# Optimization experiments

Measured on AMD Instinct MI355X. Metric: run time of the kernel, lower is better.

Reference implementation:

```python
import jax, jax.numpy as jnp
import numpy as np

B, N = 16, 128
DN0, DE0, DH = 64, 16, 128  # input node dim, input edge dim, hidden dim


def _gnn2(A, x, e, w_msg, b_msg, w_node, b_node):
    """One GNN2 layer on dense batched graphs.
    A: [B,N,N] adjacency mask, x: [B,N,Dn], e: [B,N,N,De].
    Message/new-edge: relu(Linear([x_i, x_j, e_ij])) masked by A.
    New node: relu(Linear([x, sum_j msg_ij])).
    The concat-Linear is decomposed into three matmuls to avoid
    materializing the [B,N,N,2Dn+De] concat tensor.
    """
    Dn = x.shape[-1]
    Wi, Wj, We = w_msg[:Dn], w_msg[Dn:2 * Dn], w_msg[2 * Dn:]
    xi = x @ Wi                                   # [B,N,Do]
    xj = x @ Wj                                   # [B,N,Do]
    msg = jax.nn.relu(xi[:, :, None, :] + xj[:, None, :, :] + e @ We + b_msg)
    msg = msg * A[..., None]                      # mask non-edges -> new edge_attr [B,N,N,Do]
    agg = msg.sum(axis=2)                         # scatter-sum over neighbors j -> [B,N,Do]
    Wx, Wa = w_node[:Dn], w_node[Dn:]
    x_new = jax.nn.relu(x @ Wx + agg @ Wa + b_node)
    return x_new, msg


def setup_inputs() -> dict:
    key = jax.random.key(0)
    ks = iter(jax.random.split(key, 32))
    s = 0.05
    inp = {
        "edge_index": jax.random.randint(next(ks), (B, N, N), 0, 2, dtype=jnp.int32),
        "x": jax.random.normal(next(ks), (B, N, DN0), dtype=jnp.float32),
        "edge_attr": jax.random.normal(next(ks), (B, N, N, DE0), dtype=jnp.float32),
    }
    def w(shape):
        return s * jax.random.normal(next(ks), shape, dtype=jnp.float32)
    # layer 0: node_in=64, edge_in=16 -> 128
    inp["w_msg_0"], inp["b_msg_0"] = w((2 * DN0 + DE0, DH)), w((DH,))
    inp["w_node_0"], inp["b_node_0"] = w((DN0 + DH, DH)), w((DH,))
    # layers 1,2: 128 -> 128
    for l in (1, 2):
        inp[f"w_msg_{l}"], inp[f"b_msg_{l}"] = w((2 * DH + DH, DH)), w((DH,))
        inp[f"w_node_{l}"], inp[f"b_node_{l}"] = w((DH + DH, DH)), w((DH,))
    # head mlp: 128 -> 128 -> 128 -> 1
    inp["w_h1"], inp["b_h1"] = w((DH, DH)), w((DH,))
    inp["w_h2"], inp["b_h2"] = w((DH, DH)), w((DH,))
    inp["w_h3"], inp["b_h3"] = w((DH, 1)), w((1,))
    return inp


def reference(edge_index, x, edge_attr,
              w_msg_0, b_msg_0, w_node_0, b_node_0,
              w_msg_1, b_msg_1, w_node_1, b_node_1,
              w_msg_2, b_msg_2, w_node_2, b_node_2,
              w_h1, b_h1, w_h2, b_h2, w_h3, b_h3):
    A = edge_index.astype(jnp.float32)
    x = x.astype(jnp.float32)
    # layer 0
    x, e = _gnn2(A, x, edge_attr, w_msg_0, b_msg_0, w_node_0, b_node_0)
    # middle layer with 0.5 residual blend
    x_, e_ = _gnn2(A, x, e, w_msg_1, b_msg_1, w_node_1, b_node_1)
    x = 0.5 * (x + x_)
    e = 0.5 * (e + e_)
    # last layer
    x, e = _gnn2(A, x, e, w_msg_2, b_msg_2, w_node_2, b_node_2)
    # edge_mean readout + MLP head
    h = e.mean(axis=(1, 2))                       # [B, DH]
    h = jax.nn.relu(h @ w_h1 + b_h1)
    h = jax.nn.relu(h @ w_h2 + b_h2)
    out = h @ w_h3 + b_h3                         # [B, 1]
    return out.squeeze(-1)                        # [B]
```

## Files before the change

### kernel.cpp

```cpp
#include <hip/hip_runtime.h>

constexpr int B = 16, N = 128, D = 128, DN0 = 64, DE0 = 16;

typedef _Float16 half8 __attribute__((ext_vector_type(8)));
typedef _Float16 half4 __attribute__((ext_vector_type(4)));
typedef float floatx4 __attribute__((ext_vector_type(4)));
typedef float floatx16 __attribute__((ext_vector_type(16)));

__device__ __forceinline__ void gld16(const _Float16* g, _Float16* l) {
  __builtin_amdgcn_global_load_lds(
      (const __attribute__((address_space(1))) void*)g,
      (__attribute__((address_space(3))) void*)l, 16, 0, 0);
}

__global__ __launch_bounds__(128) void k_wprep(
    const float* __restrict__ wm1, const float* __restrict__ wm2,
    _Float16* __restrict__ weT1, _Float16* __restrict__ weT2) {
  const int bid = blockIdx.x;
  const int layer = bid >> 7, c = bid & 127;
  const int k = threadIdx.x;
  const float* src = layer ? wm2 : wm1;
  _Float16* dst = layer ? weT2 : weT1;
  dst[c * D + k] = (_Float16)src[(2 * D + k) * D + c];
}

__global__ __launch_bounds__(128) void k_pre0(
    const float* __restrict__ x, const float* __restrict__ wm0,
    const float* __restrict__ bm0,
    float* __restrict__ xi0, float* __restrict__ xj0) {
  const int row = blockIdx.x;
  const int c = threadIdx.x;
  __shared__ float xr[DN0];
  if (c < DN0) xr[c] = x[row * DN0 + c];
  __syncthreads();
  float ai = bm0[c], aj = 0.f;
  #pragma unroll 8
  for (int k = 0; k < DN0; ++k) {
    const float xv = xr[k];
    ai = fmaf(xv, wm0[k * D + c], ai);
    aj = fmaf(xv, wm0[(DN0 + k) * D + c], aj);
  }
  xi0[row * D + c] = ai;
  xj0[row * D + c] = aj;
}

__global__ __launch_bounds__(256) void k_edge0(
    const int* __restrict__ ei, const float* __restrict__ eattr,
    const float* __restrict__ wm0, const float* __restrict__ x0,
    const float* __restrict__ xi0, const float* __restrict__ xj0,
    const float* __restrict__ wn0, const float* __restrict__ bn0,
    const float* __restrict__ wm1, const float* __restrict__ bm1,
    _Float16* __restrict__ msg0, float* __restrict__ x1,
    float* __restrict__ xi1, float* __restrict__ xj1) {
  const int row = blockIdx.x;
  const int b = row >> 7;
  const int t = threadIdx.x;
  const int c4 = (t & 31) * 4, jb = t >> 5;

  __shared__ float e_row[N][20];
  __shared__ float w_t[DE0][D];
  __shared__ float amask[N];
  __shared__ float xi_r[D];
  __shared__ float hp2[8][32][4];
  __shared__ float sX0[DN0], sAgg[D], sX1[D];

  const float4* esrc = (const float4*)(eattr + (size_t)row * N * DE0);
  const float4* wsrc = (const float4*)(wm0 + 2 * DN0 * D);
  #pragma unroll
  for (int u = 0; u < 2; ++u) {
    const int idx4 = u * 256 + t;
    const int j = idx4 >> 2;
    const int k4 = (idx4 & 3) * 4;
    *(float4*)&e_row[j][k4] = esrc[idx4];
    ((float4*)&w_t[0][0])[idx4] = wsrc[idx4];
  }
  if (t < N) {
    amask[t] = (float)ei[(size_t)row * N + t];
    xi_r[t] = xi0[row * D + t];
  } else if (t < N + DN0) {
    sX0[t - N] = x0[(size_t)row * DN0 + (t - N)];
  }
  __syncthreads();

  float acc[16][4] = {};
  #pragma unroll 4
  for (int k = 0; k < DE0; ++k) {
    float av[16];
    #pragma unroll
    for (int p = 0; p < 16; ++p) av[p] = e_row[jb + 8 * p][k];
    const floatx4 wv = *(const floatx4*)&w_t[k][c4];
    #pragma unroll
    for (int p = 0; p < 16; ++p)
      #pragma unroll
      for (int q = 0; q < 4; ++q)
        acc[p][q] = fmaf(av[p], wv[q], acc[p][q]);
  }

  float hq[4] = {};
  const float* xjb = xj0 + (size_t)b * N * D;
  _Float16* mrow = msg0 + (size_t)row * N * D;
  const floatx4 xiv = *(const floatx4*)&xi_r[c4];
  #pragma unroll
  for (int p = 0; p < 16; ++p) {
    const int j = jb + 8 * p;
    const float am = amask[j];
    const floatx4 xjv = *(const floatx4*)&xjb[j * D + c4];
    half4 hv;
    #pragma unroll
    for (int q = 0; q < 4; ++q) {
      float v = xiv[q] + xjv[q] + acc[p][q];
      v = fmaxf(v, 0.f) * am;
      hv[q] = (_Float16)v;
      hq[q] += v;
    }
    const int cell = (c4 >> 3) ^ (j & 15);
    *(half4*)&mrow[j * D + cell * 8 + (c4 & 7)] = hv;
  }
  #pragma unroll
  for (int q = 0; q < 4; ++q) hp2[jb][t & 31][q] = hq[q];
  __syncthreads();
  if (t < D) {
    float s = 0.f;
    #pragma unroll
    for (int g = 0; g < 8; ++g) s += hp2[g][t >> 2][t & 3];
    sAgg[t] = s;
  }
  __syncthreads();

  if (t < D) {
    const int c = t;
    float a = bn0[c];
    #pragma unroll 8
    for (int k = 0; k < DN0; ++k) a = fmaf(sX0[k], wn0[k * D + c], a);
    #pragma unroll 8
    for (int k = 0; k < D; ++k) a = fmaf(sAgg[k], wn0[(DN0 + k) * D + c], a);
    a = fmaxf(a, 0.f);
    x1[(size_t)row * D + c] = a;
    sX1[c] = a;
  }
  __syncthreads();
  if (t < D) {
    const int c = t;
    float ai = bm1[c], aj = 0.f;
    #pragma unroll 8
    for (int k = 0; k < D; ++k) {
      const float xv = sX1[k];
      ai = fmaf(xv, wm1[k * D + c], ai);
      aj = fmaf(xv, wm1[(D + k) * D + c], aj);
    }
    xi1[(size_t)row * D + c] = ai;
    xj1[(size_t)row * D + c] = aj;
  }
}

__global__ __launch_bounds__(256, 4) void k_mid(
    const int* __restrict__ ei, const _Float16* __restrict__ weT1,
    const _Float16* __restrict__ weT2,
    const float* __restrict__ xi, const float* __restrict__ xj,
    const float* __restrict__ x1,
    const float* __restrict__ wn1, const float* __restrict__ bn1,
    const float* __restrict__ wm2, const float* __restrict__ bm2,
    _Float16* __restrict__ em,
    float* __restrict__ xi2, float* __restrict__ xj2) {
  const int row = blockIdx.x;
  const int b = row >> 7;
  const int t = threadIdx.x;
  const int w = t >> 6;
  const int lane = t & 63;
  const int l31 = lane & 31;
  const int l15 = lane & 15;
  const int hl = lane >> 5;

  __shared__ _Float16 sE[N * D];
  __shared__ float sAgg[D], sX1[D], sX2[D];

  const _Float16* gsrc = em + (size_t)row * N * D;
  #pragma unroll
  for (int u = 0; u < 8; ++u) {
    const int seg = (u * 4 + w) * 512;
    gld16(gsrc + seg + lane * 8, &sE[seg]);
  }

  half8 a1[8];
  #pragma unroll
  for (int ks = 0; ks < 8; ++ks)
    a1[ks] = *(const half8*)(weT1 + (32 * w + l31) * D + 16 * ks + 8 * hl);

  floatx4 xiv[4];
  #pragma unroll
  for (int g = 0; g < 4; ++g)
    xiv[g] = *(const floatx4*)&xi[(size_t)row * D + 32 * w + 8 * g + 4 * hl];
  float am[4];
  #pragma unroll
  for (int jt = 0; jt < 4; ++jt)
    am[jt] = (float)ei[(size_t)row * N + 32 * jt + l31];
  if (t < D) sX1[t] = x1[(size_t)row * D + t];

  __syncthreads();

  const floatx16 vzero = {0.f,0.f,0.f,0.f,0.f,0.f,0.f,0.f,
                          0.f,0.f,0.f,0.f,0.f,0.f,0.f,0.f};
  floatx16 acc[4];
  #pragma unroll
  for (int jt = 0; jt < 4; ++jt) acc[jt] = vzero;
  #pragma unroll
  for (int ks = 0; ks < 8; ++ks)
    #pragma unroll
    for (int jt = 0; jt < 4; ++jt) {
      const half8 bv = *(const half8*)
          &sE[(32 * jt + l31) * D + (((2 * ks + hl) ^ l15) << 3)];
      acc[jt] = __builtin_amdgcn_mfma_f32_32x32x16_f16(a1[ks], bv, acc[jt], 0, 0, 0);
    }

  __syncthreads();

  const float* xjb = xj + (size_t)b * N * D;
  floatx4 hacc[4];
  #pragma unroll
  for (int g = 0; g < 4; ++g) hacc[g] = (floatx4){0.f, 0.f, 0.f, 0.f};
  #pragma unroll
  for (int jt = 0; jt < 4; ++jt) {
    const int j = 32 * jt + l31;
    #pragma unroll
    for (int g = 0; g < 4; ++g) {
      const int cofs = 32 * w + 8 * g + 4 * hl;
      const int hidx = j * D + (((4 * w + g) ^ l15) << 3) + 4 * hl;
      const floatx4 xjv = *(const floatx4*)&xjb[j * D + cofs];
      const half4 m0 = *(const half4*)&sE[hidx];
      half4 mid;
      floatx4 m1;
      #pragma unroll
      for (int r = 0; r < 4; ++r) {
        const float v = xiv[g][r] + xjv[r] + acc[jt][4 * g + r];
        m1[r] = fmaxf(v, 0.f) * am[jt];
        mid[r] = (_Float16)(0.5f * ((float)m0[r] + m1[r]));
      }
      *(half4*)&sE[hidx] = mid;
      hacc[g] += m1;
    }
  }

  #pragma unroll
  for (int m = 1; m < 32; m <<= 1)
    #pragma unroll
    for (int g = 0; g < 4; ++g)
      #pragma unroll
      for (int r = 0; r < 4; ++r)
        hacc[g][r] += __shfl_xor(hacc[g][r], m, 64);
  if (l31 == 0) {
    #pragma unroll
    for (int g = 0; g < 4; ++g)
      *(floatx4*)&sAgg[32 * w + 8 * g + 4 * hl] = hacc[g];
  }

  half8 a2[8];
  #pragma unroll
  for (int ks = 0; ks < 8; ++ks)
    a2[ks] = *(const half8*)(weT2 + (32 * w + l31) * D + 16 * ks + 8 * hl);

  __syncthreads();

  #pragma unroll
  for (int jt = 0; jt < 4; ++jt) acc[jt] = vzero;
  #pragma unroll
  for (int ks = 0; ks < 8; ++ks)
    #pragma unroll
    for (int jt = 0; jt < 4; ++jt) {
      const half8 bv = *(const half8*)
          &sE[(32 * jt + l31) * D + (((2 * ks + hl) ^ l15) << 3)];
      acc[jt] = __builtin_amdgcn_mfma_f32_32x32x16_f16(a2[ks], bv, acc[jt], 0, 0, 0);
    }

  __syncthreads();

  #pragma unroll
  for (int jt = 0; jt < 4; ++jt) {
    const int j = 32 * jt + l31;
    #pragma unroll
    for (int g = 0; g < 4; ++g) {
      const int hidx = j * D + (((4 * w + g) ^ l15) << 3) + 4 * hl;
      half4 tv;
      #pragma unroll
      for (int r = 0; r < 4; ++r) tv[r] = (_Float16)acc[jt][4 * g + r];
      *(half4*)&sE[hidx] = tv;
    }
  }

  __syncthreads();

  uint4* gdst = (uint4*)(em + (size_t)row * N * D);
  const uint4* ls = (const uint4*)sE;
  #pragma unroll
  for (int u = 0; u < 8; ++u) {
    const int idx4 = u * 256 + t;
    gdst[idx4] = ls[idx4];
  }

  if (t < D) {
    const int c = t;
    float a = bn1[c];
    #pragma unroll 8
    for (int k = 0; k < D; ++k) a = fmaf(sX1[k], wn1[k * D + c], a);
    #pragma unroll 8
    for (int k = 0; k < D; ++k) a = fmaf(sAgg[k], wn1[(D + k) * D + c], a);
    sX2[c] = 0.5f * (sX1[c] + fmaxf(a, 0.f));
  }
  __syncthreads();
  if (t < D) {
    const int c = t;
    float ai = bm2[c], aj = 0.f;
    #pragma unroll 8
    for (int k = 0; k < D; ++k) {
      const float xv = sX2[k];
      ai = fmaf(xv, wm2[k * D + c], ai);
      aj = fmaf(xv, wm2[(D + k) * D + c], aj);
    }
    xi2[(size_t)row * D + c] = ai;
    xj2[(size_t)row * D + c] = aj;
  }
}

__global__ __launch_bounds__(256) void k_fin(
    const int* __restrict__ ei, const _Float16* __restrict__ t2,
    const float* __restrict__ xi, const float* __restrict__ xj,
    float* __restrict__ rowsum) {
  const int row = blockIdx.x;
  const int b = row >> 7;
  const int t = threadIdx.x;
  const int c8 = (t & 15) * 8, jr = t >> 4;

  __shared__ float sMask[N];
  __shared__ float hp[16][16][8];
  if (t < N) sMask[t] = (float)ei[(size_t)row * N + t];
  float xiv[8];
  *(floatx4*)&xiv[0] = *(const floatx4*)&xi[row * D + c8];
  *(floatx4*)&xiv[4] = *(const floatx4*)&xi[row * D + c8 + 4];
  __syncthreads();

  const _Float16* src = t2 + (size_t)row * N * D;
  const float* xjb = xj + (size_t)b * N * D;
  float acc8[8] = {};
  #pragma unroll
  for (int u = 0; u < 8; ++u) {
    const int j = u * 16 + jr;
    const half8 tv = *(const half8*)(src + j * D + (((t & 15) ^ jr) << 3));
    const float am = sMask[j];
    const floatx4 xj0 = *(const floatx4*)&xjb[j * D + c8];
    const floatx4 xj1 = *(const floatx4*)&xjb[j * D + c8 + 4];
    #pragma unroll
    for (int r = 0; r < 4; ++r) {
      acc8[r]     += fmaxf(xiv[r] + xj0[r] + (float)tv[r], 0.f) * am;
      acc8[4 + r] += fmaxf(xiv[4 + r] + xj1[r] + (float)tv[4 + r], 0.f) * am;
    }
  }
  #pragma unroll
  for (int k = 0; k < 8; ++k) hp[jr][t & 15][k] = acc8[k];
  __syncthreads();
  if (t < D) {
    float s = 0.f;
    #pragma unroll
    for (int g = 0; g < 16; ++g) s += hp[g][t >> 3][t & 7];
    rowsum[row * D + t] = s;
  }
}

__global__ __launch_bounds__(128) void k_head(
    const float* __restrict__ rowsum,
    const float* __restrict__ w1, const float* __restrict__ b1,
    const float* __restrict__ w2, const float* __restrict__ b2,
    const float* __restrict__ w3, const float* __restrict__ b3,
    float* __restrict__ out) {
  const int b = blockIdx.x;
  const int c = threadIdx.x;
  __shared__ float hr[D], h1r[D], h2r[D];
  const float* rs = rowsum + (size_t)b * N * D;
  float s = 0.f;
  for (int i = 0; i < N; ++i) s += rs[i * D + c];
  hr[c] = s * (1.f / (N * N));
  __syncthreads();
  float a = b1[c];
  #pragma unroll 8
  for (int k = 0; k < D; ++k) a = fmaf(hr[k], w1[k * D + c], a);
  h1r[c] = fmaxf(a, 0.f);
  __syncthreads();
  a = b2[c];
  #pragma unroll 8
  for (int k = 0; k < D; ++k) a = fmaf(h1r[k], w2[k * D + c], a);
  h2r[c] = fmaxf(a, 0.f);
  __syncthreads();
  hr[c] = h2r[c] * w3[c];
  __syncthreads();
  if (c == 0) {
    float s2 = b3[0];
    for (int k = 0; k < D; ++k) s2 += hr[k];
    out[b] = s2;
  }
}

extern "C" void kernel_launch(void* const* d_in, const int* in_sizes, int n_in,
                              void* d_out, int out_size, void* d_ws, size_t ws_size,
                              hipStream_t stream) {
  const int*   ei  = (const int*)d_in[0];
  const float* x0  = (const float*)d_in[1];
  const float* ea  = (const float*)d_in[2];
  const float* wm0 = (const float*)d_in[3];
  const float* bm0 = (const float*)d_in[4];
  const float* wn0 = (const float*)d_in[5];
  const float* bn0 = (const float*)d_in[6];
  const float* wm1 = (const float*)d_in[7];
  const float* bm1 = (const float*)d_in[8];
  const float* wn1 = (const float*)d_in[9];
  const float* bn1 = (const float*)d_in[10];
  const float* wm2 = (const float*)d_in[11];
  const float* bm2 = (const float*)d_in[12];
  const float* wh1 = (const float*)d_in[15];
  const float* bh1 = (const float*)d_in[16];
  const float* wh2 = (const float*)d_in[17];
  const float* bh2 = (const float*)d_in[18];
  const float* wh3 = (const float*)d_in[19];
  const float* bh3 = (const float*)d_in[20];
  float* out = (float*)d_out;

  _Float16* msg0h = (_Float16*)d_ws;
  _Float16* weT1  = msg0h + (size_t)B * N * N * D;
  _Float16* weT2  = weT1 + D * D;
  float* f = (float*)(weT2 + D * D);
  size_t off = 0;
  const size_t R = (size_t)B * N * D;
  float* xi0  = f + off; off += R;
  float* xj0  = f + off; off += R;
  float* x1   = f + off; off += R;
  float* xi1  = f + off; off += R;
  float* xj1  = f + off; off += R;
  float* xi2  = f + off; off += R;
  float* xj2  = f + off; off += R;
  float* rsum = f + off; off += R;

  const int rows = B * N;
  k_wprep<<<256, 128, 0, stream>>>(wm1, wm2, weT1, weT2);
  k_pre0 <<<rows, 128, 0, stream>>>(x0, wm0, bm0, xi0, xj0);
  k_edge0<<<rows, 256, 0, stream>>>(ei, ea, wm0, x0, xi0, xj0,
                                    wn0, bn0, wm1, bm1,
                                    msg0h, x1, xi1, xj1);
  k_mid  <<<rows, 256, 0, stream>>>(ei, weT1, weT2, xi1, xj1, x1,
                                    wn1, bn1, wm2, bm2,
                                    msg0h, xi2, xj2);
  k_fin  <<<rows, 256, 0, stream>>>(ei, msg0h, xi2, xj2, rsum);
  k_head <<<B,    128, 0, stream>>>(rsum, wh1, bh1, wh2, bh2, wh3, bh3, out);
}
```

Measured before the change: 261.5 us.

## Split layer-1 node update out of k_mid into a separate k_node1 kernel

Moves the per-row node update and the layer-2 xi/xj projections out of the edge-heavy k_mid kernel into a new lightweight kernel, passing the aggregated messages through a global buffer. The aim is to keep k_mid's tail, where only half the threads ran serial FMA loops, from holding the large LDS allocation and stalling the MFMA phase of the next block. Launch bounds for k_mid also drop from 4 to 2 waves per EU, giving the compiler more register room. The cost is an extra kernel launch and a global round-trip for agg1.

```diff
diff --git a/kernel.cpp b/kernel.cpp
--- a/kernel.cpp
+++ b/kernel.cpp
@@ -153,15 +153,41 @@
   }
 }
 
-__global__ __launch_bounds__(256, 4) void k_mid(
+__global__ __launch_bounds__(128) void k_node1(
+    const float* __restrict__ x1, const float* __restrict__ agg1,
+    const float* __restrict__ wn1, const float* __restrict__ bn1,
+    const float* __restrict__ wm2, const float* __restrict__ bm2,
+    float* __restrict__ xi2, float* __restrict__ xj2) {
+  const int row = blockIdx.x;
+  const int c = threadIdx.x;
+  __shared__ float x1r[D], ar[D], x2r[D];
+  x1r[c] = x1[row * D + c];
+  ar[c] = agg1[row * D + c];
+  __syncthreads();
+  float a = bn1[c];
+  #pragma unroll 8
+  for (int k = 0; k < D; ++k) a = fmaf(x1r[k], wn1[k * D + c], a);
+  #pragma unroll 8
+  for (int k = 0; k < D; ++k) a = fmaf(ar[k], wn1[(D + k) * D + c], a);
+  x2r[c] = 0.5f * (x1r[c] + fmaxf(a, 0.f));
+  __syncthreads();
+  float ai = bm2[c], aj = 0.f;
+  #pragma unroll 8
+  for (int k = 0; k < D; ++k) {
+    const float xv = x2r[k];
+    ai = fmaf(xv, wm2[k * D + c], ai);
+    aj = fmaf(xv, wm2[(D + k) * D + c], aj);
+  }
+  xi2[row * D + c] = ai;
+  xj2[row * D + c] = aj;
+}
+
+__global__ __launch_bounds__(256, 2) void k_mid(
     const int* __restrict__ ei, const _Float16* __restrict__ weT1,
     const _Float16* __restrict__ weT2,
     const float* __restrict__ xi, const float* __restrict__ xj,
-    const float* __restrict__ x1,
-    const float* __restrict__ wn1, const float* __restrict__ bn1,
-    const float* __restrict__ wm2, const float* __restrict__ bm2,
     _Float16* __restrict__ em,
-    float* __restrict__ xi2, float* __restrict__ xj2) {
+    float* __restrict__ agg1) {
   const int row = blockIdx.x;
   const int b = row >> 7;
   const int t = threadIdx.x;
@@ -172,7 +198,6 @@
   const int hl = lane >> 5;
 
   __shared__ _Float16 sE[N * D];
-  __shared__ float sAgg[D], sX1[D], sX2[D];
 
   const _Float16* gsrc = em + (size_t)row * N * D;
   #pragma unroll
@@ -194,7 +219,6 @@
   #pragma unroll
   for (int jt = 0; jt < 4; ++jt)
     am[jt] = (float)ei[(size_t)row * N + 32 * jt + l31];
-  if (t < D) sX1[t] = x1[(size_t)row * D + t];
 
   __syncthreads();
 
@@ -250,7 +274,7 @@
   if (l31 == 0) {
     #pragma unroll
     for (int g = 0; g < 4; ++g)
-      *(floatx4*)&sAgg[32 * w + 8 * g + 4 * hl] = hacc[g];
+      *(floatx4*)&agg1[(size_t)row * D + 32 * w + 8 * g + 4 * hl] = hacc[g];
   }
 
   half8 a2[8];
@@ -294,29 +318,6 @@
   for (int u = 0; u < 8; ++u) {
     const int idx4 = u * 256 + t;
     gdst[idx4] = ls[idx4];
-  }
-
-  if (t < D) {
-    const int c = t;
-    float a = bn1[c];
-    #pragma unroll 8
-    for (int k = 0; k < D; ++k) a = fmaf(sX1[k], wn1[k * D + c], a);
-    #pragma unroll 8
-    for (int k = 0; k < D; ++k) a = fmaf(sAgg[k], wn1[(D + k) * D + c], a);
-    sX2[c] = 0.5f * (sX1[c] + fmaxf(a, 0.f));
-  }
-  __syncthreads();
-  if (t < D) {
-    const int c = t;
-    float ai = bm2[c], aj = 0.f;
-    #pragma unroll 8
-    for (int k = 0; k < D; ++k) {
-      const float xv = sX2[k];
-      ai = fmaf(xv, wm2[k * D + c], ai);
-      aj = fmaf(xv, wm2[(D + k) * D + c], aj);
-    }
-    xi2[(size_t)row * D + c] = ai;
-    xj2[(size_t)row * D + c] = aj;
   }
 }
 
@@ -432,6 +433,7 @@
   float* x1   = f + off; off += R;
   float* xi1  = f + off; off += R;
   float* xj1  = f + off; off += R;
+  float* agg1 = f + off; off += R;
   float* xi2  = f + off; off += R;
   float* xj2  = f + off; off += R;
   float* rsum = f + off; off += R;
@@ -442,9 +444,8 @@
   k_edge0<<<rows, 256, 0, stream>>>(ei, ea, wm0, x0, xi0, xj0,
                                     wn0, bn0, wm1, bm1,
                                     msg0h, x1, xi1, xj1);
-  k_mid  <<<rows, 256, 0, stream>>>(ei, weT1, weT2, xi1, xj1, x1,
-                                    wn1, bn1, wm2, bm2,
-                                    msg0h, xi2, xj2);
+  k_mid  <<<rows, 256, 0, stream>>>(ei, weT1, weT2, xi1, xj1, msg0h, agg1);
+  k_node1<<<rows, 128, 0, stream>>>(x1, agg1, wn1, bn1, wm2, bm2, xi2, xj2);
   k_fin  <<<rows, 256, 0, stream>>>(ei, msg0h, xi2, xj2, rsum);
   k_head <<<B,    128, 0, stream>>>(rsum, wh1, bh1, wh2, bh2, wh3, bh3, out);
 }
```

Measured after the change: 253.7 us. -3.0%, faster.
